# Optimization experiments

Measured on AMD Instinct MI355X. Metric: run time of the kernel, lower is better.

The kernel has to match this reference:

```python
import jax, jax.numpy as jnp
import numpy as np


def setup_inputs() -> dict:
    key = jax.random.key(0)
    kx, kd = jax.random.split(key)
    B, S, E = 32, 1024, 256
    x = jax.random.normal(kx, (B, S, E), dtype=jnp.float32)
    duration = jax.random.randint(kd, (B, S), 0, 8).astype(jnp.int64)
    return {"x": x, "duration": duration}


def reference(x, duration):
    # x: [B, S, E] float, duration: [B, S] int (mel frames per phoneme)
    B, S, E = x.shape
    cum = jnp.cumsum(duration, axis=1)          # [B, S] exclusive upper boundaries
    mel_len = cum[:, -1]                        # [B]
    max_mel = int(jnp.max(mel_len))             # pad target = batch max (matches torch)
    t = jnp.arange(max_mel)                     # [T]
    # frame t belongs to token i where cum[i-1] <= t < cum[i]; zero-duration
    # tokens are naturally skipped by side='right'.
    idx = jax.vmap(lambda c: jnp.searchsorted(c, t, side='right'))(cum)  # [B, T]
    idx = jnp.minimum(idx, S - 1)
    out = jnp.take_along_axis(x, idx[..., None], axis=1)  # [B, T, E]
    mel_mask = (t[None, :] >= mel_len[:, None]).astype(jnp.int32)  # [B, T], 1 = pad
    out = out * (1 - mel_mask)[..., None].astype(x.dtype)           # zero padded frames
    return out, mel_mask
```

## Files before the change

### kernel.cpp

```cpp
#include <hip/hip_runtime.h>

#define BB 32
#define SS 1024
#define EE 256

typedef float f4 __attribute__((ext_vector_type(4)));
typedef int   i4 __attribute__((ext_vector_type(4)));

__global__ void lr_onepass_kernel(const float* __restrict__ x,
                                  const int* __restrict__ dur,
                                  float* __restrict__ out,
                                  float* __restrict__ mask,
                                  int max_mel) {
    __shared__ int scum[SS];
    __shared__ int wtot[4];
    const int b = blockIdx.y;
    const int tid = threadIdx.x;
    const int lane = tid & 63;
    const int wave = tid >> 6;

    const i4 d = ((const i4*)(dur + b * SS))[tid];
    const int s0 = d.x;
    const int s1 = s0 + d.y;
    const int s2 = s1 + d.z;
    const int s3 = s2 + d.w;
    int inc = s3;
    for (int dd = 1; dd < 64; dd <<= 1) {
        const int y = __shfl_up(inc, dd, 64);
        if (lane >= dd) inc += y;
    }
    if (lane == 63) wtot[wave] = inc;
    __syncthreads();
    int woff = 0;
#pragma unroll
    for (int w = 0; w < 4; ++w) woff += (w < wave) ? wtot[w] : 0;
    const int toff = woff + inc - s3;
    scum[tid * 4 + 0] = toff + s0;
    scum[tid * 4 + 1] = toff + s1;
    scum[tid * 4 + 2] = toff + s2;
    scum[tid * 4 + 3] = toff + s3;
    const int mel_len = wtot[0] + wtot[1] + wtot[2] + wtot[3];
    __syncthreads();

    const int t = blockIdx.x * 4 + wave;
    f4* obase = (f4*)(out + (size_t)b * max_mel * EE);
    float* mrow = mask + (size_t)b * max_mel;

    if (t < SS) {
        const int c1 = scum[t];
        const int c0 = t ? scum[t - 1] : 0;
        if (c1 > c0) {
            const f4* xrow = (const f4*)(x + ((size_t)b * SS + t) * EE);
            const f4 v = __builtin_nontemporal_load(xrow + lane);
            for (int tt = c0; tt < c1; ++tt)
                __builtin_nontemporal_store(v, obase + (size_t)tt * (EE / 4) + lane);
            if (lane < c1 - c0) mrow[c0 + lane] = 0.0f;
        }
    }
    if (t >= mel_len && t < max_mel) {
        const f4 z = {0.f, 0.f, 0.f, 0.f};
        __builtin_nontemporal_store(z, obase + (size_t)t * (EE / 4) + lane);
        if (lane == 0) mrow[t] = 1.0f;
    }
}

extern "C" void kernel_launch(void* const* d_in, const int* in_sizes, int n_in,
                              void* d_out, int out_size, void* d_ws, size_t ws_size,
                              hipStream_t stream) {
    const float* x   = (const float*)d_in[0];
    const int*   dur = (const int*)d_in[1];
    float* out = (float*)d_out;

    const int max_mel = out_size / (BB * (EE + 1));
    float* mask = out + (size_t)BB * max_mel * EE;

    const int span = (max_mel > SS) ? max_mel : SS;
    dim3 grid((span + 3) / 4, BB);
    lr_onepass_kernel<<<grid, 256, 0, stream>>>(x, dur, out, mask, max_mel);
}
```

Baseline: 155.6 us.

## Split cumsum into separate kernel and drop per-block redundant scan

```diff
diff --git a/kernel.cpp b/kernel.cpp
--- a/kernel.cpp
+++ b/kernel.cpp
@@ -7,14 +7,9 @@
 typedef float f4 __attribute__((ext_vector_type(4)));
 typedef int   i4 __attribute__((ext_vector_type(4)));
 
-__global__ void lr_onepass_kernel(const float* __restrict__ x,
-                                  const int* __restrict__ dur,
-                                  float* __restrict__ out,
-                                  float* __restrict__ mask,
-                                  int max_mel) {
-    __shared__ int scum[SS];
+__global__ void lr_cumsum_kernel(const int* __restrict__ dur, int* __restrict__ cum) {
     __shared__ int wtot[4];
-    const int b = blockIdx.y;
+    const int b = blockIdx.x;
     const int tid = threadIdx.x;
     const int lane = tid & 63;
     const int wave = tid >> 6;
@@ -35,31 +30,39 @@
 #pragma unroll
     for (int w = 0; w < 4; ++w) woff += (w < wave) ? wtot[w] : 0;
     const int toff = woff + inc - s3;
-    scum[tid * 4 + 0] = toff + s0;
-    scum[tid * 4 + 1] = toff + s1;
-    scum[tid * 4 + 2] = toff + s2;
-    scum[tid * 4 + 3] = toff + s3;
-    const int mel_len = wtot[0] + wtot[1] + wtot[2] + wtot[3];
-    __syncthreads();
+    i4 o; o.x = toff + s0; o.y = toff + s1; o.z = toff + s2; o.w = toff + s3;
+    ((i4*)(cum + b * SS))[tid] = o;
+}
 
+__global__ void lr_fused_kernel(const float* __restrict__ x,
+                                const int* __restrict__ cum,
+                                float* __restrict__ out,
+                                float* __restrict__ mask,
+                                int max_mel) {
+    const int b = blockIdx.y;
+    const int wave = threadIdx.x >> 6;
+    const int lane = threadIdx.x & 63;
     const int t = blockIdx.x * 4 + wave;
+
+    const int* crow = cum + b * SS;
+    const int mel_len = crow[SS - 1];
     f4* obase = (f4*)(out + (size_t)b * max_mel * EE);
     float* mrow = mask + (size_t)b * max_mel;
 
     if (t < SS) {
-        const int c1 = scum[t];
-        const int c0 = t ? scum[t - 1] : 0;
+        const int c1 = crow[t];
+        const int c0 = (t == 0) ? 0 : crow[t - 1];
         if (c1 > c0) {
             const f4* xrow = (const f4*)(x + ((size_t)b * SS + t) * EE);
             const f4 v = __builtin_nontemporal_load(xrow + lane);
             for (int tt = c0; tt < c1; ++tt)
-                __builtin_nontemporal_store(v, obase + (size_t)tt * (EE / 4) + lane);
+                obase[(size_t)tt * (EE / 4) + lane] = v;
             if (lane < c1 - c0) mrow[c0 + lane] = 0.0f;
         }
     }
     if (t >= mel_len && t < max_mel) {
         const f4 z = {0.f, 0.f, 0.f, 0.f};
-        __builtin_nontemporal_store(z, obase + (size_t)t * (EE / 4) + lane);
+        obase[(size_t)t * (EE / 4) + lane] = z;
         if (lane == 0) mrow[t] = 1.0f;
     }
 }
@@ -73,8 +76,11 @@
 
     const int max_mel = out_size / (BB * (EE + 1));
     float* mask = out + (size_t)BB * max_mel * EE;
+    int* cum = (int*)d_ws;
+
+    lr_cumsum_kernel<<<BB, 256, 0, stream>>>(dur, cum);
 
     const int span = (max_mel > SS) ? max_mel : SS;
     dim3 grid((span + 3) / 4, BB);
-    lr_onepass_kernel<<<grid, 256, 0, stream>>>(x, dur, out, mask, max_mel);
+    lr_fused_kernel<<<grid, 256, 0, stream>>>(x, cum, out, mask, max_mel);
 }
```

New measurement: 144.9 us. 1.07x faster.
